# Kernel optimization log

Hardware: AMD Instinct MI355X
Metric: run time of the kernel (lower is better)

The kernel has to match this reference:

```python
import jax, jax.numpy as jnp
import numpy as np

N = 20000      # nodes
E = 640000     # edges (avg degree 32)
F = 6          # feature_dim
D = 128        # weight_dim
L = 3          # lstm num_layers
DEPTH = 10     # extra iterations after initial call


def setup_inputs() -> dict:
    key = jax.random.key(0)
    ks = jax.random.split(key, 10)
    s = 0.05
    return {
        "features": jax.random.normal(ks[0], (N, F), jnp.float32),
        "src": jax.random.randint(ks[1], (E,), 0, N),
        "dst": jax.random.randint(ks[2], (E,), 0, N),
        "W_in": jax.random.normal(ks[3], (F, D), jnp.float32) * s,
        "b_in": jnp.zeros((D,), jnp.float32),
        "Wih0": jax.random.normal(ks[4], (4 * D, 2 * D), jnp.float32) * s,   # layer 0: input = concat(h_in, feat)
        "Wih_rest": jax.random.normal(ks[5], (2, 4 * D, D), jnp.float32) * s,  # layers 1,2
        "Whh": jax.random.normal(ks[6], (L, 4 * D, D), jnp.float32) * s,
        "bih": jnp.zeros((L, 4 * D), jnp.float32),
        "bhh": jnp.zeros((L, 4 * D), jnp.float32),
        "W_out": jax.random.normal(ks[7], (D, 1), jnp.float32) * s,
        "b_out": jnp.zeros((1,), jnp.float32),
    }


def _lstm_cell(x, h, c, Wih, Whh, b):
    # PyTorch gate order: i, f, g, o
    gates = x @ Wih.T + h @ Whh.T + b              # [N, 4D]
    i, f, g, o = jnp.split(gates, 4, axis=-1)
    i = jax.nn.sigmoid(i)
    f = jax.nn.sigmoid(f)
    o = jax.nn.sigmoid(o)
    g = jnp.tanh(g)
    c_new = f * c + i * g
    h_new = o * jnp.tanh(c_new)
    return h_new, c_new


def reference(features, src, dst, W_in, b_in, Wih0, Wih_rest, Whh, bih, bhh, W_out, b_out):
    n = features.shape[0]
    b = bih + bhh                                   # [L, 4D]

    def agg(x):
        # DGL update_all(copy_src, mean): mean over incoming edges (src -> dst)
        s = jax.ops.segment_sum(x[src], dst, num_segments=n)
        deg = jax.ops.segment_sum(jnp.ones((src.shape[0],), x.dtype), dst, num_segments=n)
        return jnp.where(deg[:, None] > 0, s / jnp.maximum(deg, 1.0)[:, None], 0.0)

    feat = jax.nn.relu(features @ W_in + b_in)      # [N, D]
    h = jnp.zeros((L, n, D), features.dtype)
    c = jnp.zeros((L, n, D), features.dtype)

    def step(carry, _):
        feat, h, c = carry
        x0 = jnp.concatenate([agg(feat), feat], axis=-1)   # [N, 2D]
        h0, c0 = _lstm_cell(x0, h[0], c[0], Wih0, Whh[0], b[0])
        h1, c1 = _lstm_cell(h0, h[1], c[1], Wih_rest[0], Whh[1], b[1])
        h2, c2 = _lstm_cell(h1, h[2], c[2], Wih_rest[1], Whh[2], b[2])
        return (h2, jnp.stack([h0, h1, h2]), jnp.stack([c0, c1, c2])), None

    # initial call + depth extra iterations, all structurally identical
    (feat, h, c), _ = jax.lax.scan(step, (feat, h, c), None, length=1 + DEPTH)
    return h[-1] @ W_out + b_out                    # [N, 1]
```

## Files before the change

### kernel.cpp

```cpp
#include <hip/hip_runtime.h>
#include <math.h>

typedef _Float16 f16;
typedef __attribute__((ext_vector_type(8))) _Float16 half8;
typedef __attribute__((ext_vector_type(4))) float float4v;

__device__ __forceinline__ float fast_sigmoid(float x) { return 1.0f / (1.0f + __expf(-x)); }
__device__ __forceinline__ float fast_tanh(float x) {
    float a = fabsf(x);
    float e = __expf(-2.0f * a);
    float t = (1.0f - e) / (1.0f + e);
    return copysignf(t, x);
}

__device__ __forceinline__ void async_copy16(const void* gsrc, void* ldst) {
    __builtin_amdgcn_global_load_lds(
        (const __attribute__((address_space(1))) void*)gsrc,
        (__attribute__((address_space(3))) void*)ldst,
        16, 0, 0);
}

__global__ void packb_kernel(const float* __restrict__ Wih, int Kih,
                             const float* __restrict__ Whh, int K,
                             const float* __restrict__ bih, const float* __restrict__ bhh,
                             f16* __restrict__ Bp, float* __restrict__ bp) {
    int t = blockIdx.x * blockDim.x + threadIdx.x;
    if (t >= (K << 9)) return;
    int colp = t / K;
    int k = t - colp * K;
    int dg = colp >> 6, q = (colp >> 4) & 3, dl = colp & 15;
    int j = q * 128 + dg * 16 + dl;
    float v = (k < Kih) ? Wih[j * Kih + k] : Whh[j * (K - Kih) + (k - Kih)];
    Bp[t] = (f16)v;
    if (k == 0) bp[colp] = bih[j] + bhh[j];
}

__global__ void feat0_kernel(const float* __restrict__ features, const float* __restrict__ W_in,
                             const float* __restrict__ b_in, f16* __restrict__ feat, int n) {
    int t = blockIdx.x * blockDim.x + threadIdx.x;
    if (t >= n * 128) return;
    int node = t >> 7;
    int d = t & 127;
    float s = b_in[d];
#pragma unroll
    for (int k = 0; k < 6; ++k) s += features[node * 6 + k] * W_in[k * 128 + d];
    feat[t] = (f16)fmaxf(s, 0.0f);
}

__global__ void hist_kernel(const int* __restrict__ dst, int* __restrict__ cnt, int e) {
    int t = blockIdx.x * blockDim.x + threadIdx.x;
    if (t < e) atomicAdd(&cnt[dst[t]], 1);
}

__global__ void scan_kernel(const int* __restrict__ cnt, int* __restrict__ off,
                            int* __restrict__ cur, float* __restrict__ recip, int n) {
    __shared__ int wsum[16];
    __shared__ int stot;
    int t = threadIdx.x;
    int lane = t & 63, wv = t >> 6;
    int R = 0;
    int rounds = (n + 1023) >> 10;
    for (int i = 0; i < rounds; ++i) {
        int idx = (i << 10) + t;
        int v = (idx < n) ? cnt[idx] : 0;
        int s = v;
#pragma unroll
        for (int o = 1; o < 64; o <<= 1) {
            int u = __shfl_up(s, o, 64);
            if (lane >= o) s += u;
        }
        if (lane == 63) wsum[wv] = s;
        __syncthreads();
        if (t == 0) {
            int a = 0;
#pragma unroll
            for (int j = 0; j < 16; ++j) { int x = wsum[j]; wsum[j] = a; a += x; }
            stot = a;
        }
        __syncthreads();
        int excl = R + wsum[wv] + s - v;
        if (idx < n) {
            off[idx] = excl; cur[idx] = excl;
            recip[idx] = (v > 0) ? 1.0f / (float)v : 0.0f;
        }
        R += stot;
        __syncthreads();
    }
    if (t == 0) off[n] = R;
}

__global__ void scatter_kernel(const int* __restrict__ src, const int* __restrict__ dst,
                               int* __restrict__ cur, int* __restrict__ esrc, int e) {
    int t = blockIdx.x * blockDim.x + threadIdx.x;
    if (t >= e) return;
    int d = dst[t];
    int p = atomicAdd(&cur[d], 1);
    esrc[p] = src[t];
}

__global__ __launch_bounds__(256, 6) void agg_kernel(
    const f16* __restrict__ feat, const int* __restrict__ off,
    const int* __restrict__ esrc, const float* __restrict__ recip,
    f16* __restrict__ agg, int n) {
    int slot = threadIdx.x >> 4;
    int lane = threadIdx.x & 15;
    int v = blockIdx.x * 16 + slot;
    if (v >= n) return;
    int e0 = off[v], e1 = off[v + 1];
    int a[8];
#pragma unroll
    for (int j = 0; j < 8; ++j) a[j] = 0;
    const float SC = 1048576.0f;
    int e = e0;
    for (; e + 8 <= e1; e += 8) {
        int ss[8];
#pragma unroll
        for (int u = 0; u < 8; ++u) ss[u] = esrc[e + u];
        half8 vv[8];
#pragma unroll
        for (int u = 0; u < 8; ++u)
            vv[u] = *(const half8*)&feat[(size_t)ss[u] * 128 + lane * 8];
#pragma unroll
        for (int u = 0; u < 8; ++u)
#pragma unroll
            for (int j = 0; j < 8; ++j) a[j] += (int)((float)vv[u][j] * SC);
    }
    for (; e < e1; ++e) {
        int s = esrc[e];
        half8 v0 = *(const half8*)&feat[(size_t)s * 128 + lane * 8];
#pragma unroll
        for (int j = 0; j < 8; ++j) a[j] += (int)((float)v0[j] * SC);
    }
    float r = recip[v] * 9.5367431640625e-07f;
    half8 o;
#pragma unroll
    for (int j = 0; j < 8; ++j) o[j] = (f16)((float)a[j] * r);
    *(half8*)&agg[(size_t)v * 128 + lane * 8] = o;
}

#define BM 64

template <int PARTS>
__global__ __launch_bounds__(256, 3) void gemm_lstm(
    const f16* __restrict__ A0, const f16* __restrict__ A1, const f16* __restrict__ A2,
    const f16* __restrict__ Bp, const float* __restrict__ bp,
    float* __restrict__ c, f16* __restrict__ h_out, int nrows) {
    constexpr int K = PARTS * 128;
    __shared__ f16 As[64 * 32];
    __shared__ f16 Bs[256 * 32];

    const int tid = threadIdx.x;
    const int w = tid >> 6;
    const int lane = tid & 63;
    const int dl = lane & 15;
    const int quad = lane >> 4;
    const int row0 = blockIdx.x * BM;
    const int cb = blockIdx.y;

    float4v acc[4][4];
#pragma unroll
    for (int q = 0; q < 4; ++q) {
        float b = bp[cb * 256 + w * 64 + q * 16 + dl];
#pragma unroll
        for (int rt = 0; rt < 4; ++rt) {
            acc[rt][q][0] = b; acc[rt][q][1] = b; acc[rt][q][2] = b; acc[rt][q][3] = b;
        }
    }

    const int srow = lane >> 2;
    const int sj = lane & 3;
    const int sg = sj ^ ((srow >> 1) & 3);
    const int rslot = (quad ^ ((dl >> 1) & 3)) << 3;

    for (int kt = 0; kt < PARTS * 4; ++kt) {
        const f16* Ap = A0;
        const int pi = kt >> 2;
        if (PARTS >= 2 && pi == 1) Ap = A1;
        if (PARTS >= 3 && pi == 2) Ap = A2;
        const int kk = (kt & 3) * 32;

        __syncthreads();
        async_copy16(&Ap[(size_t)(row0 + w * 16 + srow) * 128 + kk + (sg << 3)],
                     (f16*)As + w * 512);
        const f16* Bbase = Bp + (size_t)(cb * 256) * K + kt * 32;
#pragma unroll
        for (int i = 0; i < 4; ++i) {
            int m = i * 4 + w;
            async_copy16(&Bbase[(size_t)(m * 16 + srow) * K + (sg << 3)],
                         (f16*)Bs + m * 512);
        }
        __syncthreads();

        half8 a[4], b[4];
#pragma unroll
        for (int rt = 0; rt < 4; ++rt)
            a[rt] = *(const half8*)&As[(rt * 16 + dl) * 32 + rslot];
#pragma unroll
        for (int q = 0; q < 4; ++q)
            b[q] = *(const half8*)&Bs[((w * 4 + q) * 16 + dl) * 32 + rslot];
#pragma unroll
        for (int rt = 0; rt < 4; ++rt)
#pragma unroll
            for (int q = 0; q < 4; ++q)
                acc[rt][q] = __builtin_amdgcn_mfma_f32_16x16x32_f16(a[rt], b[q], acc[rt][q], 0, 0, 0);
    }

    const int d = cb * 64 + w * 16 + dl;
#pragma unroll
    for (int rt = 0; rt < 4; ++rt) {
#pragma unroll
        for (int r = 0; r < 4; ++r) {
            int n = row0 + rt * 16 + (quad << 2) + r;
            if (n < nrows) {
                float ig = fast_sigmoid(acc[rt][0][r]);
                float fg = fast_sigmoid(acc[rt][1][r]);
                float gg = fast_tanh(acc[rt][2][r]);
                float og = fast_sigmoid(acc[rt][3][r]);
                float cold = c[(size_t)n * 128 + d];
                float cn = fg * cold + ig * gg;
                c[(size_t)n * 128 + d] = cn;
                h_out[(size_t)n * 128 + d] = (f16)(og * fast_tanh(cn));
            }
        }
    }
}

__global__ void out_kernel(const f16* __restrict__ h2, const float* __restrict__ Wout,
                           const float* __restrict__ bout, float* __restrict__ out) {
    int n = blockIdx.x;
    int l = threadIdx.x;
    float v = (float)h2[(size_t)n * 128 + l] * Wout[l] +
              (float)h2[(size_t)n * 128 + 64 + l] * Wout[64 + l];
#pragma unroll
    for (int o = 32; o > 0; o >>= 1) v += __shfl_down(v, o, 64);
    if (l == 0) out[n] = v + bout[0];
}

extern "C" void kernel_launch(void* const* d_in, const int* in_sizes, int n_in,
                              void* d_out, int out_size, void* d_ws, size_t ws_size,
                              hipStream_t stream) {
    const float* features = (const float*)d_in[0];
    const int*   src      = (const int*)d_in[1];
    const int*   dst      = (const int*)d_in[2];
    const float* W_in     = (const float*)d_in[3];
    const float* b_in     = (const float*)d_in[4];
    const float* Wih0     = (const float*)d_in[5];
    const float* Wih_rest = (const float*)d_in[6];
    const float* Whh      = (const float*)d_in[7];
    const float* bih      = (const float*)d_in[8];
    const float* bhh      = (const float*)d_in[9];
    const float* W_out    = (const float*)d_in[10];
    const float* b_out    = (const float*)d_in[11];
    float* out = (float*)d_out;

    const int N = in_sizes[0] / 6;
    const int E = in_sizes[1];
    const int NP = N + BM;

    char* ws = (char*)d_ws;
    size_t pos = 0;
    auto alloc = [&](size_t bytes) -> void* {
        void* p = ws + pos;
        pos = (pos + bytes + 255) & ~(size_t)255;
        return p;
    };
    const size_t hrow = 128;
    const size_t hbytes = (size_t)NP * hrow * sizeof(f16);
    const size_t cbytes = (size_t)NP * hrow * sizeof(float);
    f16* feath = (f16*)alloc(hbytes);
    f16* aggh  = (f16*)alloc(hbytes);
    f16* hblk  = (f16*)alloc(6 * hbytes);
    f16* hA[3], * hB[3];
    for (int l = 0; l < 3; ++l) {
        hA[l] = hblk + (size_t)l * NP * hrow;
        hB[l] = hblk + (size_t)(l + 3) * NP * hrow;
    }
    float* cblk = (float*)alloc(3 * cbytes);
    float* c0 = cblk + 0 * (size_t)NP * hrow;
    float* c1 = cblk + 1 * (size_t)NP * hrow;
    float* c2 = cblk + 2 * (size_t)NP * hrow;
    f16* Bp0 = (f16*)alloc((size_t)512 * 384 * sizeof(f16));
    f16* Bp1 = (f16*)alloc((size_t)512 * 256 * sizeof(f16));
    f16* Bp2 = (f16*)alloc((size_t)512 * 256 * sizeof(f16));
    float* bp0 = (float*)alloc(512 * sizeof(float));
    float* bp1 = (float*)alloc(512 * sizeof(float));
    float* bp2 = (float*)alloc(512 * sizeof(float));
    int*   cnt   = (int*)alloc((size_t)N * 4);
    int*   offs  = (int*)alloc((size_t)(N + 1) * 4);
    int*   cur   = (int*)alloc((size_t)N * 4);
    int*   esrc  = (int*)alloc((size_t)E * 4);
    float* recip = (float*)alloc((size_t)N * 4);

    hipMemsetAsync(hblk, 0, 6 * hbytes, stream);
    hipMemsetAsync(cblk, 0, 3 * cbytes, stream);
    hipMemsetAsync(cnt, 0, (size_t)N * 4, stream);

    packb_kernel<<<(512 * 384 + 255) / 256, 256, 0, stream>>>(
        Wih0, 256, Whh, 384, bih, bhh, Bp0, bp0);
    packb_kernel<<<(512 * 256 + 255) / 256, 256, 0, stream>>>(
        Wih_rest, 128, Whh + 512 * 128, 256, bih + 512, bhh + 512, Bp1, bp1);
    packb_kernel<<<(512 * 256 + 255) / 256, 256, 0, stream>>>(
        Wih_rest + 512 * 128, 128, Whh + 2 * 512 * 128, 256, bih + 1024, bhh + 1024, Bp2, bp2);

    feat0_kernel<<<(N * 128 + 255) / 256, 256, 0, stream>>>(features, W_in, b_in, feath, N);
    hist_kernel<<<(E + 255) / 256, 256, 0, stream>>>(dst, cnt, E);
    scan_kernel<<<1, 1024, 0, stream>>>(cnt, offs, cur, recip, N);
    scatter_kernel<<<(E + 255) / 256, 256, 0, stream>>>(src, dst, cur, esrc, E);

    const dim3 ggrid((N + BM - 1) / BM, 2, 1);
    const int gagg = (N + 15) / 16;
    const f16* featcur = feath;
    f16 *r0 = hA[0], *r1 = hA[1], *r2 = hA[2];
    f16 *w0 = hB[0], *w1 = hB[1], *w2 = hB[2];
    for (int step = 0; step < 11; ++step) {
        agg_kernel<<<gagg, 256, 0, stream>>>(featcur, offs, esrc, recip, aggh, N);
        gemm_lstm<3><<<ggrid, 256, 0, stream>>>(aggh, featcur, r0, Bp0, bp0, c0, w0, N);
        gemm_lstm<2><<<ggrid, 256, 0, stream>>>(w0, r1, nullptr, Bp1, bp1, c1, w1, N);
        gemm_lstm<2><<<ggrid, 256, 0, stream>>>(w1, r2, nullptr, Bp2, bp2, c2, w2, N);
        featcur = w2;
        f16* t;
        t = r0; r0 = w0; w0 = t;
        t = r1; r1 = w1; w1 = t;
        t = r2; r2 = w2; w2 = t;
    }
    out_kernel<<<N, 64, 0, stream>>>((const f16*)featcur, W_out, b_out, out);
}
```

Measured before the change: 1.154 ms.

## Fuse neighbor mean aggregation into layer-0 LSTM GEMM and skip zero-state work

The separate aggregation kernel is removed. Each layer-0 GEMM block now gathers and averages neighbor features for its 64 rows into shared memory and feeds them as the first K tiles, which removes the global write and read of the aggregated buffer and one launch per step. The first step gets template variants that skip the Whh·h K-tiles and the old-c read, since the initial state is zero, so the memsets of h and c are dropped. The cost is that both column-block CTAs (grid y=2) redo the same gather, and the gather now runs inside a GEMM kernel with lower occupancy and less unrolling, which may hide memory latency worse.

After: 1.336 ms. 15.8% more time.

```diff
diff --git a/kernel.cpp b/kernel.cpp
--- a/kernel.cpp
+++ b/kernel.cpp
@@ -4,6 +4,9 @@
 typedef _Float16 f16;
 typedef __attribute__((ext_vector_type(8))) _Float16 half8;
 typedef __attribute__((ext_vector_type(4))) float float4v;
+
+#define SC_INT 1048576.0f
+#define SC_INV 9.5367431640625e-07f
 
 __device__ __forceinline__ float fast_sigmoid(float x) { return 1.0f / (1.0f + __expf(-x)); }
 __device__ __forceinline__ float fast_tanh(float x) {
@@ -98,54 +101,18 @@
     esrc[p] = src[t];
 }
 
-__global__ __launch_bounds__(256, 6) void agg_kernel(
-    const f16* __restrict__ feat, const int* __restrict__ off,
-    const int* __restrict__ esrc, const float* __restrict__ recip,
-    f16* __restrict__ agg, int n) {
-    int slot = threadIdx.x >> 4;
-    int lane = threadIdx.x & 15;
-    int v = blockIdx.x * 16 + slot;
-    if (v >= n) return;
-    int e0 = off[v], e1 = off[v + 1];
-    int a[8];
-#pragma unroll
-    for (int j = 0; j < 8; ++j) a[j] = 0;
-    const float SC = 1048576.0f;
-    int e = e0;
-    for (; e + 8 <= e1; e += 8) {
-        int ss[8];
-#pragma unroll
-        for (int u = 0; u < 8; ++u) ss[u] = esrc[e + u];
-        half8 vv[8];
-#pragma unroll
-        for (int u = 0; u < 8; ++u)
-            vv[u] = *(const half8*)&feat[(size_t)ss[u] * 128 + lane * 8];
-#pragma unroll
-        for (int u = 0; u < 8; ++u)
-#pragma unroll
-            for (int j = 0; j < 8; ++j) a[j] += (int)((float)vv[u][j] * SC);
-    }
-    for (; e < e1; ++e) {
-        int s = esrc[e];
-        half8 v0 = *(const half8*)&feat[(size_t)s * 128 + lane * 8];
-#pragma unroll
-        for (int j = 0; j < 8; ++j) a[j] += (int)((float)v0[j] * SC);
-    }
-    float r = recip[v] * 9.5367431640625e-07f;
-    half8 o;
-#pragma unroll
-    for (int j = 0; j < 8; ++j) o[j] = (f16)((float)a[j] * r);
-    *(half8*)&agg[(size_t)v * 128 + lane * 8] = o;
-}
-
 #define BM 64
 
-template <int PARTS>
-__global__ __launch_bounds__(256, 3) void gemm_lstm(
-    const f16* __restrict__ A0, const f16* __restrict__ A1, const f16* __restrict__ A2,
+template <bool FIRST>
+__global__ __launch_bounds__(256, 3) void gemm_lstm0(
+    const f16* __restrict__ feat, const f16* __restrict__ hprev,
+    const int* __restrict__ off, const int* __restrict__ esrc,
+    const float* __restrict__ recip,
     const f16* __restrict__ Bp, const float* __restrict__ bp,
     float* __restrict__ c, f16* __restrict__ h_out, int nrows) {
-    constexpr int K = PARTS * 128;
+    constexpr int K = 384;
+    constexpr int KT = FIRST ? 8 : 12;
+    __shared__ f16 Agg[64 * 136];
     __shared__ f16 As[64 * 32];
     __shared__ f16 Bs[256 * 32];
 
@@ -157,6 +124,45 @@
     const int row0 = blockIdx.x * BM;
     const int cb = blockIdx.y;
 
+    {
+        const int slot = tid >> 4;
+        const int ln = tid & 15;
+        for (int sweep = 0; sweep < 4; ++sweep) {
+            const int r = sweep * 16 + slot;
+            const int v = row0 + r;
+            int a[8];
+#pragma unroll
+            for (int j = 0; j < 8; ++j) a[j] = 0;
+            float rr = 0.0f;
+            if (v < nrows) {
+                int e0 = off[v], e1 = off[v + 1];
+                rr = recip[v] * SC_INV;
+                int e = e0;
+                for (; e + 4 <= e1; e += 4) {
+                    int s0 = esrc[e], s1 = esrc[e + 1], s2 = esrc[e + 2], s3 = esrc[e + 3];
+                    half8 v0 = *(const half8*)&feat[(size_t)s0 * 128 + ln * 8];
+                    half8 v1 = *(const half8*)&feat[(size_t)s1 * 128 + ln * 8];
+                    half8 v2 = *(const half8*)&feat[(size_t)s2 * 128 + ln * 8];
+                    half8 v3 = *(const half8*)&feat[(size_t)s3 * 128 + ln * 8];
+#pragma unroll
+                    for (int j = 0; j < 8; ++j)
+                        a[j] += (int)((float)v0[j] * SC_INT) + (int)((float)v1[j] * SC_INT)
+                              + (int)((float)v2[j] * SC_INT) + (int)((float)v3[j] * SC_INT);
+                }
+                for (; e < e1; ++e) {
+                    int s = esrc[e];
+                    half8 v0 = *(const half8*)&feat[(size_t)s * 128 + ln * 8];
+#pragma unroll
+                    for (int j = 0; j < 8; ++j) a[j] += (int)((float)v0[j] * SC_INT);
+                }
+            }
+            half8 o;
+#pragma unroll
+            for (int j = 0; j < 8; ++j) o[j] = (f16)((float)a[j] * rr);
+            *(half8*)&Agg[r * 136 + ln * 8] = o;
+        }
+    }
+
     float4v acc[4][4];
 #pragma unroll
     for (int q = 0; q < 4; ++q) {
@@ -172,16 +178,14 @@
     const int sg = sj ^ ((srow >> 1) & 3);
     const int rslot = (quad ^ ((dl >> 1) & 3)) << 3;
 
-    for (int kt = 0; kt < PARTS * 4; ++kt) {
-        const f16* Ap = A0;
-        const int pi = kt >> 2;
-        if (PARTS >= 2 && pi == 1) Ap = A1;
-        if (PARTS >= 3 && pi == 2) Ap = A2;
-        const int kk = (kt & 3) * 32;
-
-        __syncthreads();
-        async_copy16(&Ap[(size_t)(row0 + w * 16 + srow) * 128 + kk + (sg << 3)],
-                     (f16*)As + w * 512);
+    for (int kt = 0; kt < KT; ++kt) {
+        __syncthreads();
+        if (kt >= 4) {
+            const f16* Ap = (kt < 8) ? feat : hprev;
+            const int kk = (kt & 3) * 32;
+            async_copy16(&Ap[(size_t)(row0 + w * 16 + srow) * 128 + kk + (sg << 3)],
+                         (f16*)As + w * 512);
+        }
         const f16* Bbase = Bp + (size_t)(cb * 256) * K + kt * 32;
 #pragma unroll
         for (int i = 0; i < 4; ++i) {
@@ -192,9 +196,15 @@
         __syncthreads();
 
         half8 a[4], b[4];
-#pragma unroll
-        for (int rt = 0; rt < 4; ++rt)
-            a[rt] = *(const half8*)&As[(rt * 16 + dl) * 32 + rslot];
+        if (kt < 4) {
+#pragma unroll
+            for (int rt = 0; rt < 4; ++rt)
+                a[rt] = *(const half8*)&Agg[(rt * 16 + dl) * 136 + kt * 32 + (quad << 3)];
+        } else {
+#pragma unroll
+            for (int rt = 0; rt < 4; ++rt)
+                a[rt] = *(const half8*)&As[(rt * 16 + dl) * 32 + rslot];
+        }
 #pragma unroll
         for (int q = 0; q < 4; ++q)
             b[q] = *(const half8*)&Bs[((w * 4 + q) * 16 + dl) * 32 + rslot];
@@ -216,7 +226,90 @@
                 float fg = fast_sigmoid(acc[rt][1][r]);
                 float gg = fast_tanh(acc[rt][2][r]);
                 float og = fast_sigmoid(acc[rt][3][r]);
-                float cold = c[(size_t)n * 128 + d];
+                float cold = FIRST ? 0.0f : c[(size_t)n * 128 + d];
+                float cn = fg * cold + ig * gg;
+                c[(size_t)n * 128 + d] = cn;
+                h_out[(size_t)n * 128 + d] = (f16)(og * fast_tanh(cn));
+            }
+        }
+    }
+}
+
+template <bool FIRST>
+__global__ __launch_bounds__(256, 3) void gemm_lstm12(
+    const f16* __restrict__ A0, const f16* __restrict__ A1,
+    const f16* __restrict__ Bp, const float* __restrict__ bp,
+    float* __restrict__ c, f16* __restrict__ h_out, int nrows) {
+    constexpr int K = 256;
+    constexpr int KT = FIRST ? 4 : 8;
+    __shared__ f16 As[64 * 32];
+    __shared__ f16 Bs[256 * 32];
+
+    const int tid = threadIdx.x;
+    const int w = tid >> 6;
+    const int lane = tid & 63;
+    const int dl = lane & 15;
+    const int quad = lane >> 4;
+    const int row0 = blockIdx.x * BM;
+    const int cb = blockIdx.y;
+
+    float4v acc[4][4];
+#pragma unroll
+    for (int q = 0; q < 4; ++q) {
+        float b = bp[cb * 256 + w * 64 + q * 16 + dl];
+#pragma unroll
+        for (int rt = 0; rt < 4; ++rt) {
+            acc[rt][q][0] = b; acc[rt][q][1] = b; acc[rt][q][2] = b; acc[rt][q][3] = b;
+        }
+    }
+
+    const int srow = lane >> 2;
+    const int sj = lane & 3;
+    const int sg = sj ^ ((srow >> 1) & 3);
+    const int rslot = (quad ^ ((dl >> 1) & 3)) << 3;
+
+    for (int kt = 0; kt < KT; ++kt) {
+        const f16* Ap = (kt < 4) ? A0 : A1;
+        const int kk = (kt & 3) * 32;
+
+        __syncthreads();
+        async_copy16(&Ap[(size_t)(row0 + w * 16 + srow) * 128 + kk + (sg << 3)],
+                     (f16*)As + w * 512);
+        const f16* Bbase = Bp + (size_t)(cb * 256) * K + kt * 32;
+#pragma unroll
+        for (int i = 0; i < 4; ++i) {
+            int m = i * 4 + w;
+            async_copy16(&Bbase[(size_t)(m * 16 + srow) * K + (sg << 3)],
+                         (f16*)Bs + m * 512);
+        }
+        __syncthreads();
+
+        half8 a[4], b[4];
+#pragma unroll
+        for (int rt = 0; rt < 4; ++rt)
+            a[rt] = *(const half8*)&As[(rt * 16 + dl) * 32 + rslot];
+#pragma unroll
+        for (int q = 0; q < 4; ++q)
+            b[q] = *(const half8*)&Bs[((w * 4 + q) * 16 + dl) * 32 + rslot];
+#pragma unroll
+        for (int rt = 0; rt < 4; ++rt)
+#pragma unroll
+            for (int q = 0; q < 4; ++q)
+                acc[rt][q] = __builtin_amdgcn_mfma_f32_16x16x32_f16(a[rt], b[q], acc[rt][q], 0, 0, 0);
+    }
+
+    const int d = cb * 64 + w * 16 + dl;
+#pragma unroll
+    for (int rt = 0; rt < 4; ++rt) {
+#pragma unroll
+        for (int r = 0; r < 4; ++r) {
+            int n = row0 + rt * 16 + (quad << 2) + r;
+            if (n < nrows) {
+                float ig = fast_sigmoid(acc[rt][0][r]);
+                float fg = fast_sigmoid(acc[rt][1][r]);
+                float gg = fast_tanh(acc[rt][2][r]);
+                float og = fast_sigmoid(acc[rt][3][r]);
+                float cold = FIRST ? 0.0f : c[(size_t)n * 128 + d];
                 float cn = fg * cold + ig * gg;
                 c[(size_t)n * 128 + d] = cn;
                 h_out[(size_t)n * 128 + d] = (f16)(og * fast_tanh(cn));
@@ -268,7 +361,6 @@
     const size_t hbytes = (size_t)NP * hrow * sizeof(f16);
     const size_t cbytes = (size_t)NP * hrow * sizeof(float);
     f16* feath = (f16*)alloc(hbytes);
-    f16* aggh  = (f16*)alloc(hbytes);
     f16* hblk  = (f16*)alloc(6 * hbytes);
     f16* hA[3], * hB[3];
     for (int l = 0; l < 3; ++l) {
@@ -291,8 +383,6 @@
     int*   esrc  = (int*)alloc((size_t)E * 4);
     float* recip = (float*)alloc((size_t)N * 4);
 
-    hipMemsetAsync(hblk, 0, 6 * hbytes, stream);
-    hipMemsetAsync(cblk, 0, 3 * cbytes, stream);
     hipMemsetAsync(cnt, 0, (size_t)N * 4, stream);
 
     packb_kernel<<<(512 * 384 + 255) / 256, 256, 0, stream>>>(
@@ -308,15 +398,21 @@
     scatter_kernel<<<(E + 255) / 256, 256, 0, stream>>>(src, dst, cur, esrc, E);
 
     const dim3 ggrid((N + BM - 1) / BM, 2, 1);
-    const int gagg = (N + 15) / 16;
-    const f16* featcur = feath;
     f16 *r0 = hA[0], *r1 = hA[1], *r2 = hA[2];
     f16 *w0 = hB[0], *w1 = hB[1], *w2 = hB[2];
-    for (int step = 0; step < 11; ++step) {
-        agg_kernel<<<gagg, 256, 0, stream>>>(featcur, offs, esrc, recip, aggh, N);
-        gemm_lstm<3><<<ggrid, 256, 0, stream>>>(aggh, featcur, r0, Bp0, bp0, c0, w0, N);
-        gemm_lstm<2><<<ggrid, 256, 0, stream>>>(w0, r1, nullptr, Bp1, bp1, c1, w1, N);
-        gemm_lstm<2><<<ggrid, 256, 0, stream>>>(w1, r2, nullptr, Bp2, bp2, c2, w2, N);
+
+    gemm_lstm0<true><<<ggrid, 256, 0, stream>>>(feath, nullptr, offs, esrc, recip,
+                                                Bp0, bp0, c0, w0, N);
+    gemm_lstm12<true><<<ggrid, 256, 0, stream>>>(w0, nullptr, Bp1, bp1, c1, w1, N);
+    gemm_lstm12<true><<<ggrid, 256, 0, stream>>>(w1, nullptr, Bp2, bp2, c2, w2, N);
+    const f16* featcur = w2;
+    { f16* t; t = r0; r0 = w0; w0 = t; t = r1; r1 = w1; w1 = t; t = r2; r2 = w2; w2 = t; }
+
+    for (int step = 1; step < 11; ++step) {
+        gemm_lstm0<false><<<ggrid, 256, 0, stream>>>(featcur, r0, offs, esrc, recip,
+                                                     Bp0, bp0, c0, w0, N);
+        gemm_lstm12<false><<<ggrid, 256, 0, stream>>>(w0, r1, Bp1, bp1, c1, w1, N);
+        gemm_lstm12<false><<<ggrid, 256, 0, stream>>>(w1, r2, Bp2, bp2, c2, w2, N);
         featcur = w2;
         f16* t;
         t = r0; r0 = w0; w0 = t;
```
